# Optimization experiments

Hardware: AMD Instinct MI355X
Metric: run time of the kernel (lower is better)

## Reference

```python
import math
import jax, jax.numpy as jnp
import numpy as np

DIM = 1024
HEADS = 16
KV_HEADS = 4            # use_mqa: heads // 4
HEAD_DIM = DIM // HEADS  # 64
KV_DIM = KV_HEADS * HEAD_DIM  # 256
WINDOW = 64
SCALE = HEAD_DIM ** -0.5


def _alibi_slopes(n_heads: int) -> np.ndarray:
    # n_heads is a power of 2 here
    start = 2.0 ** (-(2.0 ** (-(math.log2(n_heads) - 3))))
    return np.array([start * (start ** i) for i in range(n_heads)], dtype=np.float32)


def setup_inputs() -> dict:
    key = jax.random.key(0)
    ks = jax.random.split(key, 5)
    B, N = 1, 2048
    x = jax.random.normal(ks[0], (B, N, DIM), dtype=jnp.float32)
    # Linear weights stored as [in, out] (applied as x @ W)
    sq = 1.0 / math.sqrt(DIM)
    Wq = jax.random.uniform(ks[1], (DIM, DIM), jnp.float32, -sq, sq)
    Wk = jax.random.uniform(ks[2], (DIM, KV_DIM), jnp.float32, -sq, sq)
    Wv = jax.random.uniform(ks[3], (DIM, KV_DIM), jnp.float32, -sq, sq)
    Wo = jax.random.uniform(ks[4], (DIM, DIM), jnp.float32, -sq, sq)
    return {"x": x, "Wq": Wq, "Wk": Wk, "Wv": Wv, "Wo": Wo}


def reference(x, Wq, Wk, Wv, Wo):
    B, N, C = x.shape
    # projections -> [B, H, N, hd]
    q = (x @ Wq).reshape(B, N, HEADS, HEAD_DIM).transpose(0, 2, 1, 3)
    k = (x @ Wk).reshape(B, N, KV_HEADS, HEAD_DIM).transpose(0, 2, 1, 3)
    v = (x @ Wv).reshape(B, N, KV_HEADS, HEAD_DIM).transpose(0, 2, 1, 3)
    # MQA: repeat kv heads (torch repeat_interleave on head dim)
    rep = HEADS // KV_HEADS
    k = jnp.repeat(k, rep, axis=1)
    v = jnp.repeat(v, rep, axis=1)

    scores = jnp.einsum("bhqd,bhkd->bhqk", q, k) * SCALE  # [B,H,N,N]

    # ALiBi bias: distance[i, j] = j - i, scaled per head
    idx = jnp.arange(N)
    dist = (idx[None, :] - idx[:, None]).astype(scores.dtype)  # [N, N]
    slopes = jnp.asarray(_alibi_slopes(HEADS))                 # [H]
    scores = scores + dist[None, None, :, :] * slopes[None, :, None, None]

    # causal AND local band (|i-j| <= WINDOW) -> allowed iff j in [i-WINDOW, i]
    causal = idx[None, :] <= idx[:, None]
    band = jnp.abs(idx[:, None] - idx[None, :]) <= WINDOW
    allowed = causal & band  # [N, N]
    scores_local = jnp.where(allowed[None, None], scores, -jnp.inf)
    attn_local = jax.nn.softmax(scores_local, axis=-1)
    out_local = jnp.einsum("bhqk,bhkd->bhqd", attn_local, v)

    # global: strided keys every WINDOW positions, full (non-causal) softmax
    k_g = k[:, :, ::WINDOW, :]
    v_g = v[:, :, ::WINDOW, :]
    scores_g = jnp.einsum("bhqd,bhkd->bhqk", q, k_g) * SCALE
    attn_g = jax.nn.softmax(scores_g, axis=-1)
    out_global = jnp.einsum("bhqk,bhkd->bhqd", attn_g, v_g)

    out = (out_local + out_global).transpose(0, 2, 1, 3).reshape(B, N, C)
    return out @ Wo
```

## Files before the change

### kernel.cpp

```cpp
#include <hip/hip_runtime.h>

#define SCALE 0.125f

typedef unsigned short ushort_t;
typedef unsigned short ushortx8 __attribute__((ext_vector_type(8)));
typedef unsigned short ushortx4 __attribute__((ext_vector_type(4)));
typedef short bf16x8 __attribute__((ext_vector_type(8)));
typedef float f32x4 __attribute__((ext_vector_type(4)));

__device__ inline ushort_t f2bf(float f) {
  unsigned int u = __float_as_uint(f);
  u += 0x7FFFu + ((u >> 16) & 1u);
  return (ushort_t)(u >> 16);
}
__device__ inline float bf2f(ushort_t u) {
  return __uint_as_float(((unsigned int)u) << 16);
}

__global__ __launch_bounds__(256) void prep_kernel(
    const float* __restrict__ x, const float* __restrict__ Wq, const float* __restrict__ Wk,
    const float* __restrict__ Wv, const float* __restrict__ Wo,
    ushort_t* __restrict__ x_bf, ushort_t* __restrict__ wqkv_t, ushort_t* __restrict__ wo_t)
{
  __shared__ float t[64][65];
  int bid = blockIdx.x;
  const int tid = threadIdx.x;
  if (bid < 2048) {
    int idx = (bid * 256 + tid) * 4;
    if (idx < 2048 * 1024) {
      float4 f = *(const float4*)(x + idx);
      ushortx4 o = { f2bf(f.x), f2bf(f.y), f2bf(f.z), f2bf(f.w) };
      *(ushortx4*)(x_bf + idx) = o;
    }
    return;
  }
  bid -= 2048;
  const float* src; int C; ushort_t* dst; int row_off, cb, kb;
  if (bid < 256)      { src = Wq; C = 1024; dst = wqkv_t; row_off = 0;    cb = bid & 15; kb = bid >> 4; }
  else if (bid < 320) { int j = bid - 256; src = Wk; C = 256; dst = wqkv_t; row_off = 1024; cb = j & 3; kb = j >> 2; }
  else if (bid < 384) { int j = bid - 320; src = Wv; C = 256; dst = wqkv_t; row_off = 1280; cb = j & 3; kb = j >> 2; }
  else                { int j = bid - 384; src = Wo; C = 1024; dst = wo_t; row_off = 0;    cb = j & 15; kb = j >> 4; }
  const int c0 = cb * 64, k0 = kb * 64;
  const int c = tid & 63, r4 = tid >> 6;
  for (int rr = r4; rr < 64; rr += 4)
    t[c][rr] = src[(size_t)(k0 + rr) * C + c0 + c];
  __syncthreads();
  const int kk = tid & 63, n4 = tid >> 6;
  for (int nn = n4; nn < 64; nn += 4)
    dst[(size_t)(row_off + c0 + nn) * 1024 + k0 + kk] = f2bf(t[nn][kk]);
}

__global__ __launch_bounds__(256) void gemm64_kernel(
    const ushort_t* __restrict__ A, const ushort_t* __restrict__ Bt, int mode, int ntn,
    ushort_t* __restrict__ qout, ushort_t* __restrict__ kout, ushort_t* __restrict__ vout,
    float* __restrict__ fout)
{
  __shared__ __align__(16) ushort_t lA[64 * 64];
  __shared__ __align__(16) ushort_t lB[64 * 64];
  const int bid = blockIdx.x;
  const int xcd = bid & 7, g = bid >> 3;
  const int m0 = (xcd + 8 * (g / ntn)) * 64;
  const int n0 = (g % ntn) * 64;

  const int tid = threadIdx.x;
  const int lane = tid & 63, w = tid >> 6;
  const int quad = lane >> 4, l16 = lane & 15;
  const int rw = (w >> 1) * 32, cw = (w & 1) * 32;

  const int rs = tid >> 3;
  const int swz = (tid & 7) ^ (rs & 7);
  const int eL = tid * 8;
  const ushort_t* Ab = A + (size_t)(m0 + rs) * 1024 + swz * 8;
  const ushort_t* Bb = Bt + (size_t)(n0 + rs) * 1024 + swz * 8;

  const int xa = l16 & 7;
  f32x4 acc[2][2] = {};

  for (int k0 = 0; k0 < 1024; k0 += 64) {
    __syncthreads();
    __builtin_amdgcn_global_load_lds(
        (const __attribute__((address_space(1))) unsigned int*)(Ab + k0),
        (__attribute__((address_space(3))) unsigned int*)(lA + eL), 16, 0, 0);
    __builtin_amdgcn_global_load_lds(
        (const __attribute__((address_space(1))) unsigned int*)(Ab + 32 * 1024 + k0),
        (__attribute__((address_space(3))) unsigned int*)(lA + eL + 2048), 16, 0, 0);
    __builtin_amdgcn_global_load_lds(
        (const __attribute__((address_space(1))) unsigned int*)(Bb + k0),
        (__attribute__((address_space(3))) unsigned int*)(lB + eL), 16, 0, 0);
    __builtin_amdgcn_global_load_lds(
        (const __attribute__((address_space(1))) unsigned int*)(Bb + 32 * 1024 + k0),
        (__attribute__((address_space(3))) unsigned int*)(lB + eL + 2048), 16, 0, 0);
    __syncthreads();

#pragma unroll
    for (int kh = 0; kh < 2; ++kh) {
      bf16x8 a0 = *(const bf16x8*)(lA + (rw + l16) * 64      + (((kh * 4 + quad) ^ xa) << 3));
      bf16x8 a1 = *(const bf16x8*)(lA + (rw + 16 + l16) * 64 + (((kh * 4 + quad) ^ xa) << 3));
      bf16x8 b0 = *(const bf16x8*)(lB + (cw + l16) * 64      + (((kh * 4 + quad) ^ xa) << 3));
      bf16x8 b1 = *(const bf16x8*)(lB + (cw + 16 + l16) * 64 + (((kh * 4 + quad) ^ xa) << 3));
      acc[0][0] = __builtin_amdgcn_mfma_f32_16x16x32_bf16(a0, b0, acc[0][0], 0, 0, 0);
      acc[0][1] = __builtin_amdgcn_mfma_f32_16x16x32_bf16(a0, b1, acc[0][1], 0, 0, 0);
      acc[1][0] = __builtin_amdgcn_mfma_f32_16x16x32_bf16(a1, b0, acc[1][0], 0, 0, 0);
      acc[1][1] = __builtin_amdgcn_mfma_f32_16x16x32_bf16(a1, b1, acc[1][1], 0, 0, 0);
    }
  }

#pragma unroll
  for (int mg = 0; mg < 2; ++mg)
#pragma unroll
    for (int ng = 0; ng < 2; ++ng)
#pragma unroll
      for (int r = 0; r < 4; ++r) {
        const int row = m0 + rw + mg * 16 + quad * 4 + r;
        const int col = n0 + cw + ng * 16 + l16;
        const float v = acc[mg][ng][r];
        if (mode == 0) {
          if (n0 < 1024)       qout[(size_t)row * 1024 + col] = f2bf(v);
          else if (n0 < 1280)  kout[(size_t)row * 256 + (col - 1024)] = f2bf(v);
          else                 vout[(size_t)row * 256 + (col - 1280)] = f2bf(v);
        } else {
          fout[(size_t)row * 1024 + col] = v;
        }
      }
}

__global__ __launch_bounds__(256) void attn_mfma_kernel(
    const ushort_t* __restrict__ Q, const ushort_t* __restrict__ Kb,
    const ushort_t* __restrict__ Vb, ushort_t* __restrict__ O)
{
  __shared__ __align__(16) ushort_t lK[128 * 64];
  __shared__ __align__(16) ushort_t lVt[64 * 128];
  __shared__ __align__(16) ushort_t lKg[32 * 64];
  __shared__ __align__(16) ushort_t lVtg[64 * 40];
  __shared__ __align__(16) ushort_t lP[64 * 128];
  __shared__ __align__(16) ushort_t lPg[64 * 40];

  const int h = blockIdx.x, qb = blockIdx.y;
  const int tid = threadIdx.x;
  const int kvcol = (h >> 2) * 64;
  const int kbase = qb * 64 - 64;

  for (int cidx = tid; cidx < 1024; cidx += 256) {
    const int key = cidx >> 3, ch = cidx & 7;
    const int kpos = kbase + key;
    ushortx8 kv = {0,0,0,0,0,0,0,0}, vv = {0,0,0,0,0,0,0,0};
    if (kpos >= 0) {
      kv = *(const ushortx8*)(Kb + (size_t)kpos * 256 + kvcol + ch * 8);
      vv = *(const ushortx8*)(Vb + (size_t)kpos * 256 + kvcol + ch * 8);
    }
    *(ushortx8*)(lK + key * 64 + ((ch ^ (key & 7)) << 3)) = kv;
    const int kc = key >> 3, ke = key & 7;
#pragma unroll
    for (int e = 0; e < 8; ++e) {
      int dim = ch * 8 + e;
      lVt[dim * 128 + ((kc ^ (dim & 7)) << 3) + ke] = vv[e];
    }
  }
  {
    const int gk = tid >> 3, ch = tid & 7;
    const int kpos = gk * 64;
    ushortx8 kv = *(const ushortx8*)(Kb + (size_t)kpos * 256 + kvcol + ch * 8);
    ushortx8 vv = *(const ushortx8*)(Vb + (size_t)kpos * 256 + kvcol + ch * 8);
    *(ushortx8*)(lKg + gk * 64 + ((ch ^ (gk & 7)) << 3)) = kv;
#pragma unroll
    for (int e = 0; e < 8; ++e) lVtg[(ch * 8 + e) * 40 + gk] = vv[e];
  }
  __syncthreads();

  const int lane = tid & 63, w = tid >> 6;
  const int quad = lane >> 4, l16 = lane & 15;
  const int l7 = l16 & 7;
  const float slope = exp2f(-0.5f * (float)(h + 1));

  const int qrow = qb * 64 + w * 16 + l16;
  const ushort_t* qptr = Q + (size_t)qrow * 1024 + h * 64 + quad * 8;
  const bf16x8 aq0 = *(const bf16x8*)(qptr);
  const bf16x8 aq1 = *(const bf16x8*)(qptr + 32);

  float s[8][4];
#pragma unroll
  for (int kt = 0; kt < 8; ++kt) {
    const int key = kt * 16 + l16;
    const bf16x8 b0 = *(const bf16x8*)(lK + key * 64 + ((quad ^ l7) << 3));
    const bf16x8 b1 = *(const bf16x8*)(lK + key * 64 + (((4 + quad) ^ l7) << 3));
    f32x4 acc = {0.f, 0.f, 0.f, 0.f};
    acc = __builtin_amdgcn_mfma_f32_16x16x32_bf16(aq0, b0, acc, 0, 0, 0);
    acc = __builtin_amdgcn_mfma_f32_16x16x32_bf16(aq1, b1, acc, 0, 0, 0);
    const int kpos = kbase + key;
#pragma unroll
    for (int r = 0; r < 4; ++r) {
      const int qp = qb * 64 + w * 16 + quad * 4 + r;
      const int d = kpos - qp;
      const bool ok = (d <= 0) && (d >= -64) && (kpos >= 0);
      s[kt][r] = ok ? acc[r] * SCALE + (float)d * slope : -1e30f;
    }
  }
  float mr[4] = {-1e30f, -1e30f, -1e30f, -1e30f};
#pragma unroll
  for (int kt = 0; kt < 8; ++kt)
#pragma unroll
    for (int r = 0; r < 4; ++r) mr[r] = fmaxf(mr[r], s[kt][r]);
#pragma unroll
  for (int r = 0; r < 4; ++r) {
    mr[r] = fmaxf(mr[r], __shfl_xor(mr[r], 1));
    mr[r] = fmaxf(mr[r], __shfl_xor(mr[r], 2));
    mr[r] = fmaxf(mr[r], __shfl_xor(mr[r], 4));
    mr[r] = fmaxf(mr[r], __shfl_xor(mr[r], 8));
  }
  float lr[4] = {0.f, 0.f, 0.f, 0.f};
#pragma unroll
  for (int kt = 0; kt < 8; ++kt)
#pragma unroll
    for (int r = 0; r < 4; ++r) { float p = __expf(s[kt][r] - mr[r]); s[kt][r] = p; lr[r] += p; }
#pragma unroll
  for (int r = 0; r < 4; ++r) {
    lr[r] += __shfl_xor(lr[r], 1);
    lr[r] += __shfl_xor(lr[r], 2);
    lr[r] += __shfl_xor(lr[r], 4);
    lr[r] += __shfl_xor(lr[r], 8);
    lr[r] = 1.f / lr[r];
  }
#pragma unroll
  for (int kt = 0; kt < 8; ++kt) {
    const int kc = kt * 2 + (l16 >> 3);
#pragma unroll
    for (int r = 0; r < 4; ++r) {
      const int qr = w * 16 + quad * 4 + r;
      lP[qr * 128 + ((kc ^ (qr & 7)) << 3) + l7] = f2bf(s[kt][r] * lr[r]);
    }
  }

  float sg[2][4];
#pragma unroll
  for (int g16 = 0; g16 < 2; ++g16) {
    const int key = g16 * 16 + l16;
    const bf16x8 b0 = *(const bf16x8*)(lKg + key * 64 + ((quad ^ l7) << 3));
    const bf16x8 b1 = *(const bf16x8*)(lKg + key * 64 + (((4 + quad) ^ l7) << 3));
    f32x4 acc = {0.f, 0.f, 0.f, 0.f};
    acc = __builtin_amdgcn_mfma_f32_16x16x32_bf16(aq0, b0, acc, 0, 0, 0);
    acc = __builtin_amdgcn_mfma_f32_16x16x32_bf16(aq1, b1, acc, 0, 0, 0);
#pragma unroll
    for (int r = 0; r < 4; ++r) sg[g16][r] = acc[r] * SCALE;
  }
  float mg[4], lg[4];
#pragma unroll
  for (int r = 0; r < 4; ++r) {
    mg[r] = fmaxf(sg[0][r], sg[1][r]);
    mg[r] = fmaxf(mg[r], __shfl_xor(mg[r], 1));
    mg[r] = fmaxf(mg[r], __shfl_xor(mg[r], 2));
    mg[r] = fmaxf(mg[r], __shfl_xor(mg[r], 4));
    mg[r] = fmaxf(mg[r], __shfl_xor(mg[r], 8));
  }
#pragma unroll
  for (int r = 0; r < 4; ++r) {
    float p0 = __expf(sg[0][r] - mg[r]);
    float p1 = __expf(sg[1][r] - mg[r]);
    sg[0][r] = p0; sg[1][r] = p1;
    lg[r] = p0 + p1;
    lg[r] += __shfl_xor(lg[r], 1);
    lg[r] += __shfl_xor(lg[r], 2);
    lg[r] += __shfl_xor(lg[r], 4);
    lg[r] += __shfl_xor(lg[r], 8);
    lg[r] = 1.f / lg[r];
  }
#pragma unroll
  for (int g16 = 0; g16 < 2; ++g16)
#pragma unroll
    for (int r = 0; r < 4; ++r) {
      const int qr = w * 16 + quad * 4 + r;
      lPg[qr * 40 + g16 * 16 + l16] = f2bf(sg[g16][r] * lg[r]);
    }

  f32x4 acco[4] = {};
  const int qA = w * 16 + l16;
#pragma unroll
  for (int kki = 0; kki < 4; ++kki) {
    const bf16x8 ap = *(const bf16x8*)(lP + qA * 128 + (((kki * 4 + quad) ^ l7) << 3));
#pragma unroll
    for (int nt = 0; nt < 4; ++nt) {
      const int dim = nt * 16 + l16;
      const bf16x8 bv = *(const bf16x8*)(lVt + dim * 128 + (((kki * 4 + quad) ^ l7) << 3));
      acco[nt] = __builtin_amdgcn_mfma_f32_16x16x32_bf16(ap, bv, acco[nt], 0, 0, 0);
    }
  }
  {
    const bf16x8 apg = *(const bf16x8*)(lPg + qA * 40 + quad * 8);
#pragma unroll
    for (int nt = 0; nt < 4; ++nt) {
      const bf16x8 bvg = *(const bf16x8*)(lVtg + (nt * 16 + l16) * 40 + quad * 8);
      acco[nt] = __builtin_amdgcn_mfma_f32_16x16x32_bf16(apg, bvg, acco[nt], 0, 0, 0);
    }
  }
#pragma unroll
  for (int nt = 0; nt < 4; ++nt)
#pragma unroll
    for (int r = 0; r < 4; ++r) {
      const int qp = qb * 64 + w * 16 + quad * 4 + r;
      O[(size_t)qp * 1024 + h * 64 + nt * 16 + l16] = f2bf(acco[nt][r]);
    }
}

extern "C" void kernel_launch(void* const* d_in, const int* in_sizes, int n_in,
                              void* d_out, int out_size, void* d_ws, size_t ws_size,
                              hipStream_t stream)
{
  const float* x  = (const float*)d_in[0];
  const float* Wq = (const float*)d_in[1];
  const float* Wk = (const float*)d_in[2];
  const float* Wv = (const float*)d_in[3];
  const float* Wo = (const float*)d_in[4];
  float* out = (float*)d_out;

  char* ws = (char*)d_ws;
  ushort_t* x_bf   = (ushort_t*)(ws);
  ushort_t* wqkv_t = (ushort_t*)(ws + (4ull  << 20));
  ushort_t* wo_t   = (ushort_t*)(ws + (7ull  << 20));
  ushort_t* q_bf   = (ushort_t*)(ws + (9ull  << 20));
  ushort_t* k_bf   = (ushort_t*)(ws + (13ull << 20));
  ushort_t* v_bf   = (ushort_t*)(ws + (14ull << 20));
  ushort_t* at_bf  = (ushort_t*)(ws + (15ull << 20));

  prep_kernel<<<2688, 256, 0, stream>>>(x, Wq, Wk, Wv, Wo, x_bf, wqkv_t, wo_t);
  gemm64_kernel<<<768, 256, 0, stream>>>(x_bf, wqkv_t, 0, 24, q_bf, k_bf, v_bf, nullptr);
  attn_mfma_kernel<<<dim3(16, 32), 256, 0, stream>>>(q_bf, k_bf, v_bf, at_bf);
  gemm64_kernel<<<512, 256, 0, stream>>>(at_bf, wo_t, 1, 16, nullptr, nullptr, nullptr, out);
}
```

Before: 109.9 us.

## Replace LDS-staged GEMM with single-wave direct-from-global MFMA tile kernel

Both projection GEMMs now run as one 64-thread wave per 64x64 output tile. Each lane loads bf16x8 fragments of A and B straight from global memory into registers and runs a 4x4 grid of MFMA accumulators, with no LDS staging and no barriers. This removes the shared-memory round trip and __syncthreads overhead. In exchange, each tile gets only a quarter of the threads, register pressure rises (64 accumulator floats per lane), and global loads are 16-byte strided row reads that rely on L2/L1 for reuse, which can lower occupancy and latency hiding.

```diff
diff --git a/kernel.cpp b/kernel.cpp
--- a/kernel.cpp
+++ b/kernel.cpp
@@ -50,70 +50,47 @@
     dst[(size_t)(row_off + c0 + nn) * 1024 + k0 + kk] = f2bf(t[nn][kk]);
 }
 
-__global__ __launch_bounds__(256) void gemm64_kernel(
+__global__ __launch_bounds__(64) void gemm_direct_kernel(
     const ushort_t* __restrict__ A, const ushort_t* __restrict__ Bt, int mode, int ntn,
     ushort_t* __restrict__ qout, ushort_t* __restrict__ kout, ushort_t* __restrict__ vout,
     float* __restrict__ fout)
 {
-  __shared__ __align__(16) ushort_t lA[64 * 64];
-  __shared__ __align__(16) ushort_t lB[64 * 64];
   const int bid = blockIdx.x;
   const int xcd = bid & 7, g = bid >> 3;
   const int m0 = (xcd + 8 * (g / ntn)) * 64;
   const int n0 = (g % ntn) * 64;
-
-  const int tid = threadIdx.x;
-  const int lane = tid & 63, w = tid >> 6;
+  const int lane = threadIdx.x;
   const int quad = lane >> 4, l16 = lane & 15;
-  const int rw = (w >> 1) * 32, cw = (w & 1) * 32;
-
-  const int rs = tid >> 3;
-  const int swz = (tid & 7) ^ (rs & 7);
-  const int eL = tid * 8;
-  const ushort_t* Ab = A + (size_t)(m0 + rs) * 1024 + swz * 8;
-  const ushort_t* Bb = Bt + (size_t)(n0 + rs) * 1024 + swz * 8;
-
-  const int xa = l16 & 7;
-  f32x4 acc[2][2] = {};
-
-  for (int k0 = 0; k0 < 1024; k0 += 64) {
-    __syncthreads();
-    __builtin_amdgcn_global_load_lds(
-        (const __attribute__((address_space(1))) unsigned int*)(Ab + k0),
-        (__attribute__((address_space(3))) unsigned int*)(lA + eL), 16, 0, 0);
-    __builtin_amdgcn_global_load_lds(
-        (const __attribute__((address_space(1))) unsigned int*)(Ab + 32 * 1024 + k0),
-        (__attribute__((address_space(3))) unsigned int*)(lA + eL + 2048), 16, 0, 0);
-    __builtin_amdgcn_global_load_lds(
-        (const __attribute__((address_space(1))) unsigned int*)(Bb + k0),
-        (__attribute__((address_space(3))) unsigned int*)(lB + eL), 16, 0, 0);
-    __builtin_amdgcn_global_load_lds(
-        (const __attribute__((address_space(1))) unsigned int*)(Bb + 32 * 1024 + k0),
-        (__attribute__((address_space(3))) unsigned int*)(lB + eL + 2048), 16, 0, 0);
-    __syncthreads();
-
-#pragma unroll
-    for (int kh = 0; kh < 2; ++kh) {
-      bf16x8 a0 = *(const bf16x8*)(lA + (rw + l16) * 64      + (((kh * 4 + quad) ^ xa) << 3));
-      bf16x8 a1 = *(const bf16x8*)(lA + (rw + 16 + l16) * 64 + (((kh * 4 + quad) ^ xa) << 3));
-      bf16x8 b0 = *(const bf16x8*)(lB + (cw + l16) * 64      + (((kh * 4 + quad) ^ xa) << 3));
-      bf16x8 b1 = *(const bf16x8*)(lB + (cw + 16 + l16) * 64 + (((kh * 4 + quad) ^ xa) << 3));
-      acc[0][0] = __builtin_amdgcn_mfma_f32_16x16x32_bf16(a0, b0, acc[0][0], 0, 0, 0);
-      acc[0][1] = __builtin_amdgcn_mfma_f32_16x16x32_bf16(a0, b1, acc[0][1], 0, 0, 0);
-      acc[1][0] = __builtin_amdgcn_mfma_f32_16x16x32_bf16(a1, b0, acc[1][0], 0, 0, 0);
-      acc[1][1] = __builtin_amdgcn_mfma_f32_16x16x32_bf16(a1, b1, acc[1][1], 0, 0, 0);
-    }
-  }
-
-#pragma unroll
-  for (int mg = 0; mg < 2; ++mg)
-#pragma unroll
-    for (int ng = 0; ng < 2; ++ng)
+
+  const ushort_t* Ap = A + (size_t)(m0 + l16) * 1024 + quad * 8;
+  const ushort_t* Bp = Bt + (size_t)(n0 + l16) * 1024 + quad * 8;
+
+  f32x4 acc[4][4] = {};
+
+#pragma unroll 4
+  for (int k0 = 0; k0 < 1024; k0 += 32) {
+    bf16x8 af[4], bfr[4];
+#pragma unroll
+    for (int i = 0; i < 4; ++i) {
+      af[i]  = *(const bf16x8*)(Ap + (size_t)i * 16 * 1024 + k0);
+      bfr[i] = *(const bf16x8*)(Bp + (size_t)i * 16 * 1024 + k0);
+    }
+#pragma unroll
+    for (int mi = 0; mi < 4; ++mi)
+#pragma unroll
+      for (int ni = 0; ni < 4; ++ni)
+        acc[mi][ni] = __builtin_amdgcn_mfma_f32_16x16x32_bf16(af[mi], bfr[ni], acc[mi][ni], 0, 0, 0);
+  }
+
+#pragma unroll
+  for (int mi = 0; mi < 4; ++mi)
+#pragma unroll
+    for (int ni = 0; ni < 4; ++ni)
 #pragma unroll
       for (int r = 0; r < 4; ++r) {
-        const int row = m0 + rw + mg * 16 + quad * 4 + r;
-        const int col = n0 + cw + ng * 16 + l16;
-        const float v = acc[mg][ng][r];
+        const int row = m0 + mi * 16 + quad * 4 + r;
+        const int col = n0 + ni * 16 + l16;
+        const float v = acc[mi][ni][r];
         if (mode == 0) {
           if (n0 < 1024)       qout[(size_t)row * 1024 + col] = f2bf(v);
           else if (n0 < 1280)  kout[(size_t)row * 256 + (col - 1024)] = f2bf(v);
@@ -321,7 +298,7 @@
   ushort_t* at_bf  = (ushort_t*)(ws + (15ull << 20));
 
   prep_kernel<<<2688, 256, 0, stream>>>(x, Wq, Wk, Wv, Wo, x_bf, wqkv_t, wo_t);
-  gemm64_kernel<<<768, 256, 0, stream>>>(x_bf, wqkv_t, 0, 24, q_bf, k_bf, v_bf, nullptr);
+  gemm_direct_kernel<<<768, 64, 0, stream>>>(x_bf, wqkv_t, 0, 24, q_bf, k_bf, v_bf, nullptr);
   attn_mfma_kernel<<<dim3(16, 32), 256, 0, stream>>>(q_bf, k_bf, v_bf, at_bf);
-  gemm64_kernel<<<512, 256, 0, stream>>>(at_bf, wo_t, 1, 16, nullptr, nullptr, nullptr, out);
-}
+  gemm_direct_kernel<<<512, 64, 0, stream>>>(at_bf, wo_t, 1, 16, nullptr, nullptr, nullptr, out);
+}
```

Measured after the change: 144.7 us. 1.32x slower.

## Double-buffer LDS tiles in projection GEMMs to overlap loads with MFMA

Applied to the files above, without the earlier changes.

The bf16 GEMM kernel used for the QKV and output projections now keeps two LDS buffers for the A and B tiles. It issues the global-to-LDS loads for the next K slice before computing on the current one, and uses one barrier per iteration instead of two. The aim is to hide global load latency behind the MFMA work and cut barrier stalls. In exchange, LDS use per block doubles to 32KB, which may lower occupancy, and the overlap depends on where the compiler places its vmcnt waits.

```diff
diff --git a/kernel.cpp b/kernel.cpp
--- a/kernel.cpp
+++ b/kernel.cpp
@@ -50,13 +50,13 @@
     dst[(size_t)(row_off + c0 + nn) * 1024 + k0 + kk] = f2bf(t[nn][kk]);
 }
 
-__global__ __launch_bounds__(256) void gemm64_kernel(
+__global__ __launch_bounds__(256) void gemm_dbuf_kernel(
     const ushort_t* __restrict__ A, const ushort_t* __restrict__ Bt, int mode, int ntn,
     ushort_t* __restrict__ qout, ushort_t* __restrict__ kout, ushort_t* __restrict__ vout,
     float* __restrict__ fout)
 {
-  __shared__ __align__(16) ushort_t lA[64 * 64];
-  __shared__ __align__(16) ushort_t lB[64 * 64];
+  __shared__ __align__(16) ushort_t lA[2 * 64 * 64];
+  __shared__ __align__(16) ushort_t lB[2 * 64 * 64];
   const int bid = blockIdx.x;
   const int xcd = bid & 7, g = bid >> 3;
   const int m0 = (xcd + 8 * (g / ntn)) * 64;
@@ -76,34 +76,43 @@
   const int xa = l16 & 7;
   f32x4 acc[2][2] = {};
 
-  for (int k0 = 0; k0 < 1024; k0 += 64) {
+#define STAGE(buf, k0)                                                                        \
+  do {                                                                                        \
+    const int off = (buf) * 4096;                                                             \
+    __builtin_amdgcn_global_load_lds(                                                         \
+        (const __attribute__((address_space(1))) unsigned int*)(Ab + (k0)),                   \
+        (__attribute__((address_space(3))) unsigned int*)(lA + off + eL), 16, 0, 0);          \
+    __builtin_amdgcn_global_load_lds(                                                         \
+        (const __attribute__((address_space(1))) unsigned int*)(Ab + 32 * 1024 + (k0)),       \
+        (__attribute__((address_space(3))) unsigned int*)(lA + off + eL + 2048), 16, 0, 0);   \
+    __builtin_amdgcn_global_load_lds(                                                         \
+        (const __attribute__((address_space(1))) unsigned int*)(Bb + (k0)),                   \
+        (__attribute__((address_space(3))) unsigned int*)(lB + off + eL), 16, 0, 0);          \
+    __builtin_amdgcn_global_load_lds(                                                         \
+        (const __attribute__((address_space(1))) unsigned int*)(Bb + 32 * 1024 + (k0)),       \
+        (__attribute__((address_space(3))) unsigned int*)(lB + off + eL + 2048), 16, 0, 0);   \
+  } while (0)
+
+  STAGE(0, 0);
+
+  for (int it = 0; it < 16; ++it) {
+    const int cur = it & 1;
     __syncthreads();
-    __builtin_amdgcn_global_load_lds(
-        (const __attribute__((address_space(1))) unsigned int*)(Ab + k0),
-        (__attribute__((address_space(3))) unsigned int*)(lA + eL), 16, 0, 0);
-    __builtin_amdgcn_global_load_lds(
-        (const __attribute__((address_space(1))) unsigned int*)(Ab + 32 * 1024 + k0),
-        (__attribute__((address_space(3))) unsigned int*)(lA + eL + 2048), 16, 0, 0);
-    __builtin_amdgcn_global_load_lds(
-        (const __attribute__((address_space(1))) unsigned int*)(Bb + k0),
-        (__attribute__((address_space(3))) unsigned int*)(lB + eL), 16, 0, 0);
-    __builtin_amdgcn_global_load_lds(
-        (const __attribute__((address_space(1))) unsigned int*)(Bb + 32 * 1024 + k0),
-        (__attribute__((address_space(3))) unsigned int*)(lB + eL + 2048), 16, 0, 0);
-    __syncthreads();
-
+    if (it + 1 < 16) STAGE(cur ^ 1, (it + 1) * 64);
+    const int off = cur * 4096;
 #pragma unroll
     for (int kh = 0; kh < 2; ++kh) {
-      bf16x8 a0 = *(const bf16x8*)(lA + (rw + l16) * 64      + (((kh * 4 + quad) ^ xa) << 3));
-      bf16x8 a1 = *(const bf16x8*)(lA + (rw + 16 + l16) * 64 + (((kh * 4 + quad) ^ xa) << 3));
-      bf16x8 b0 = *(const bf16x8*)(lB + (cw + l16) * 64      + (((kh * 4 + quad) ^ xa) << 3));
-      bf16x8 b1 = *(const bf16x8*)(lB + (cw + 16 + l16) * 64 + (((kh * 4 + quad) ^ xa) << 3));
+      bf16x8 a0 = *(const bf16x8*)(lA + off + (rw + l16) * 64      + (((kh * 4 + quad) ^ xa) << 3));
+      bf16x8 a1 = *(const bf16x8*)(lA + off + (rw + 16 + l16) * 64 + (((kh * 4 + quad) ^ xa) << 3));
+      bf16x8 b0 = *(const bf16x8*)(lB + off + (cw + l16) * 64      + (((kh * 4 + quad) ^ xa) << 3));
+      bf16x8 b1 = *(const bf16x8*)(lB + off + (cw + 16 + l16) * 64 + (((kh * 4 + quad) ^ xa) << 3));
       acc[0][0] = __builtin_amdgcn_mfma_f32_16x16x32_bf16(a0, b0, acc[0][0], 0, 0, 0);
       acc[0][1] = __builtin_amdgcn_mfma_f32_16x16x32_bf16(a0, b1, acc[0][1], 0, 0, 0);
       acc[1][0] = __builtin_amdgcn_mfma_f32_16x16x32_bf16(a1, b0, acc[1][0], 0, 0, 0);
       acc[1][1] = __builtin_amdgcn_mfma_f32_16x16x32_bf16(a1, b1, acc[1][1], 0, 0, 0);
     }
   }
+#undef STAGE
 
 #pragma unroll
   for (int mg = 0; mg < 2; ++mg)
@@ -321,7 +330,7 @@
   ushort_t* at_bf  = (ushort_t*)(ws + (15ull << 20));
 
   prep_kernel<<<2688, 256, 0, stream>>>(x, Wq, Wk, Wv, Wo, x_bf, wqkv_t, wo_t);
-  gemm64_kernel<<<768, 256, 0, stream>>>(x_bf, wqkv_t, 0, 24, q_bf, k_bf, v_bf, nullptr);
+  gemm_dbuf_kernel<<<768, 256, 0, stream>>>(x_bf, wqkv_t, 0, 24, q_bf, k_bf, v_bf, nullptr);
   attn_mfma_kernel<<<dim3(16, 32), 256, 0, stream>>>(q_bf, k_bf, v_bf, at_bf);
-  gemm64_kernel<<<512, 256, 0, stream>>>(at_bf, wo_t, 1, 16, nullptr, nullptr, nullptr, out);
-}
+  gemm_dbuf_kernel<<<512, 256, 0, stream>>>(at_bf, wo_t, 1, 16, nullptr, nullptr, nullptr, out);
+}
```

Result: slower. 115.7 us (+5.2%).

## Split-K both projection GEMMs in two halves with separate reduction kernels

Applied to the files above, without the earlier changes.

Both GEMMs now split the K=1024 reduction into two halves, which doubles the block count (1536 and 1024 blocks) and writes fp32 partial sums to workspace. New reduce kernels add the two partials and convert to bf16 Q/K/V, or to the fp32 output. This is meant to raise occupancy and CU utilization on the 256-CU device. The cost is extra global traffic for the fp32 partials (about 12 MB and 8 MB written and read back) plus two more kernel launches.

```diff
diff --git a/kernel.cpp b/kernel.cpp
--- a/kernel.cpp
+++ b/kernel.cpp
@@ -50,17 +50,19 @@
     dst[(size_t)(row_off + c0 + nn) * 1024 + k0 + kk] = f2bf(t[nn][kk]);
 }
 
-__global__ __launch_bounds__(256) void gemm64_kernel(
-    const ushort_t* __restrict__ A, const ushort_t* __restrict__ Bt, int mode, int ntn,
-    ushort_t* __restrict__ qout, ushort_t* __restrict__ kout, ushort_t* __restrict__ vout,
-    float* __restrict__ fout)
+__global__ __launch_bounds__(256) void gemm_sk_kernel(
+    const ushort_t* __restrict__ A, const ushort_t* __restrict__ Bt, int ntile, int ntn, int N,
+    float* __restrict__ pout)
 {
   __shared__ __align__(16) ushort_t lA[64 * 64];
   __shared__ __align__(16) ushort_t lB[64 * 64];
-  const int bid = blockIdx.x;
+  int bid = blockIdx.x;
+  const int kh = bid >= ntile ? 1 : 0;
+  bid -= kh * ntile;
   const int xcd = bid & 7, g = bid >> 3;
   const int m0 = (xcd + 8 * (g / ntn)) * 64;
   const int n0 = (g % ntn) * 64;
+  const int ks = kh * 512;
 
   const int tid = threadIdx.x;
   const int lane = tid & 63, w = tid >> 6;
@@ -76,7 +78,7 @@
   const int xa = l16 & 7;
   f32x4 acc[2][2] = {};
 
-  for (int k0 = 0; k0 < 1024; k0 += 64) {
+  for (int k0 = ks; k0 < ks + 512; k0 += 64) {
     __syncthreads();
     __builtin_amdgcn_global_load_lds(
         (const __attribute__((address_space(1))) unsigned int*)(Ab + k0),
@@ -93,11 +95,11 @@
     __syncthreads();
 
 #pragma unroll
-    for (int kh = 0; kh < 2; ++kh) {
-      bf16x8 a0 = *(const bf16x8*)(lA + (rw + l16) * 64      + (((kh * 4 + quad) ^ xa) << 3));
-      bf16x8 a1 = *(const bf16x8*)(lA + (rw + 16 + l16) * 64 + (((kh * 4 + quad) ^ xa) << 3));
-      bf16x8 b0 = *(const bf16x8*)(lB + (cw + l16) * 64      + (((kh * 4 + quad) ^ xa) << 3));
-      bf16x8 b1 = *(const bf16x8*)(lB + (cw + 16 + l16) * 64 + (((kh * 4 + quad) ^ xa) << 3));
+    for (int khh = 0; khh < 2; ++khh) {
+      bf16x8 a0 = *(const bf16x8*)(lA + (rw + l16) * 64      + (((khh * 4 + quad) ^ xa) << 3));
+      bf16x8 a1 = *(const bf16x8*)(lA + (rw + 16 + l16) * 64 + (((khh * 4 + quad) ^ xa) << 3));
+      bf16x8 b0 = *(const bf16x8*)(lB + (cw + l16) * 64      + (((khh * 4 + quad) ^ xa) << 3));
+      bf16x8 b1 = *(const bf16x8*)(lB + (cw + 16 + l16) * 64 + (((khh * 4 + quad) ^ xa) << 3));
       acc[0][0] = __builtin_amdgcn_mfma_f32_16x16x32_bf16(a0, b0, acc[0][0], 0, 0, 0);
       acc[0][1] = __builtin_amdgcn_mfma_f32_16x16x32_bf16(a0, b1, acc[0][1], 0, 0, 0);
       acc[1][0] = __builtin_amdgcn_mfma_f32_16x16x32_bf16(a1, b0, acc[1][0], 0, 0, 0);
@@ -105,6 +107,7 @@
     }
   }
 
+  float* po = pout + (size_t)kh * 2048 * N;
 #pragma unroll
   for (int mg = 0; mg < 2; ++mg)
 #pragma unroll
@@ -113,15 +116,33 @@
       for (int r = 0; r < 4; ++r) {
         const int row = m0 + rw + mg * 16 + quad * 4 + r;
         const int col = n0 + cw + ng * 16 + l16;
-        const float v = acc[mg][ng][r];
-        if (mode == 0) {
-          if (n0 < 1024)       qout[(size_t)row * 1024 + col] = f2bf(v);
-          else if (n0 < 1280)  kout[(size_t)row * 256 + (col - 1024)] = f2bf(v);
-          else                 vout[(size_t)row * 256 + (col - 1280)] = f2bf(v);
-        } else {
-          fout[(size_t)row * 1024 + col] = v;
-        }
+        po[(size_t)row * N + col] = acc[mg][ng][r];
       }
+}
+
+__global__ __launch_bounds__(192) void qkv_reduce_kernel(
+    const float* __restrict__ p, ushort_t* __restrict__ qout,
+    ushort_t* __restrict__ kout, ushort_t* __restrict__ vout)
+{
+  const int row = blockIdx.x;
+  const int col = blockIdx.y * 768 + threadIdx.x * 4;
+  const size_t idx = (size_t)row * 1536 + col;
+  float4 a = *(const float4*)(p + idx);
+  float4 b = *(const float4*)(p + 2048 * 1536 + idx);
+  ushortx4 o = { f2bf(a.x + b.x), f2bf(a.y + b.y), f2bf(a.z + b.z), f2bf(a.w + b.w) };
+  if (col < 1024)      *(ushortx4*)(qout + (size_t)row * 1024 + col) = o;
+  else if (col < 1280) *(ushortx4*)(kout + (size_t)row * 256 + (col - 1024)) = o;
+  else                 *(ushortx4*)(vout + (size_t)row * 256 + (col - 1280)) = o;
+}
+
+__global__ __launch_bounds__(256) void out_reduce_kernel(
+    const float* __restrict__ p, float* __restrict__ out)
+{
+  const size_t idx = ((size_t)blockIdx.x * 256 + threadIdx.x) * 4;
+  float4 a = *(const float4*)(p + idx);
+  float4 b = *(const float4*)(p + 2048 * 1024 + idx);
+  float4 o = { a.x + b.x, a.y + b.y, a.z + b.z, a.w + b.w };
+  *(float4*)(out + idx) = o;
 }
 
 __global__ __launch_bounds__(256) void attn_mfma_kernel(
@@ -319,9 +340,13 @@
   ushort_t* k_bf   = (ushort_t*)(ws + (13ull << 20));
   ushort_t* v_bf   = (ushort_t*)(ws + (14ull << 20));
   ushort_t* at_bf  = (ushort_t*)(ws + (15ull << 20));
+  float*    pqkv   = (float*)(ws + (20ull << 20));
+  float*    pout   = (float*)(ws + (48ull << 20));
 
   prep_kernel<<<2688, 256, 0, stream>>>(x, Wq, Wk, Wv, Wo, x_bf, wqkv_t, wo_t);
-  gemm64_kernel<<<768, 256, 0, stream>>>(x_bf, wqkv_t, 0, 24, q_bf, k_bf, v_bf, nullptr);
+  gemm_sk_kernel<<<1536, 256, 0, stream>>>(x_bf, wqkv_t, 768, 24, 1536, pqkv);
+  qkv_reduce_kernel<<<dim3(2048, 2), 192, 0, stream>>>(pqkv, q_bf, k_bf, v_bf);
   attn_mfma_kernel<<<dim3(16, 32), 256, 0, stream>>>(q_bf, k_bf, v_bf, at_bf);
-  gemm64_kernel<<<512, 256, 0, stream>>>(at_bf, wo_t, 1, 16, nullptr, nullptr, nullptr, out);
-}
+  gemm_sk_kernel<<<1024, 256, 0, stream>>>(at_bf, wo_t, 512, 16, 1024, pout);
+  out_reduce_kernel<<<2048, 256, 0, stream>>>(pout, out);
+}
```

After: 116.1 us. +5.6%, slower.
